# Optimization experiments

Hardware: AMD Instinct MI355X
Metric: run time of the kernel (lower is better)

Reference implementation:

```python
import jax, jax.numpy as jnp
import numpy as np

B, T, U, V = 8, 128, 100, 1024
BLANK = 0
NEG = -1e30  # safe -inf surrogate (finite grads through logaddexp)


def setup_inputs() -> dict:
    key = jax.random.key(0)
    k1, k2 = jax.random.split(key)
    logits = jax.random.normal(k1, (B, T, U + 1, V), dtype=jnp.float32)
    # targets drawn from non-blank ids [1, V)
    targets = jax.random.randint(k2, (B, U), 1, V, dtype=jnp.int32)
    logit_lengths = jnp.full((B,), T, dtype=jnp.int32)
    target_lengths = jnp.full((B,), U, dtype=jnp.int32)
    return {"logits": logits, "targets": targets,
            "logit_lengths": logit_lengths, "target_lengths": target_lengths}


def _rnnt_nll(log_probs, targets, t_len, u_len):
    """Negative log-likelihood of one utterance.
    log_probs: [T, U+1, V] (log-softmaxed joiner output), targets: [U] int.
    alpha[t,u] = logaddexp(alpha[t-1,u] + blank[t-1,u], alpha[t,u-1] + emit[t,u-1]).
    """
    blank_lp = log_probs[:, :, BLANK]                      # [T, U+1]
    emit_lp = log_probs[:, jnp.arange(U), targets]         # [T, U]

    # row t=0: pure emissions
    alpha0 = jnp.concatenate([jnp.zeros((1,), log_probs.dtype),
                              jnp.cumsum(emit_lp[0])])     # [U+1]

    def combine(x, y):
        # linear log-space recurrence x[u] = logaddexp(c[u], x[u-1] + a[u])
        a1, c1 = x
        a2, c2 = y
        return (a1 + a2, jnp.logaddexp(c2, c1 + a2))

    def step(prev_row, inp):
        blank_prev, emit_t = inp                           # [U+1], [U]
        c = prev_row + blank_prev                          # vertical (blank) moves
        a = jnp.concatenate([jnp.full((1,), NEG, log_probs.dtype), emit_t])
        _, row = jax.lax.associative_scan(combine, (a, c))
        return row, row

    _, rows = jax.lax.scan(step, alpha0, (blank_lp[:-1], emit_lp[1:]))
    alpha = jnp.concatenate([alpha0[None, :], rows], axis=0)  # [T, U+1]

    ll = alpha[t_len - 1, u_len] + blank_lp[t_len - 1, u_len]
    return -ll


def reference(logits, targets, logit_lengths, target_lengths):
    log_probs = jax.nn.log_softmax(logits, axis=-1)
    # module passes src_lengths - 1 to rnnt_loss
    t_lens = logit_lengths - 1
    nll = jax.vmap(_rnnt_nll)(log_probs, targets, t_lens, target_lengths)
    return jnp.mean(nll)  # reduction='mean'
```

## Files before the change

kernel.cpp:

```cpp
#include <hip/hip_runtime.h>


constexpr int Bb = 8;
constexpr int Tt = 128;
constexpr int Uu = 100;
constexpr int Vv = 1024;
constexpr int UP1 = Uu + 1;
constexpr int DROWS = 244;
constexpr int PAIRS = 52;
constexpr int ROWB  = PAIRS * 8;
constexpr int LROWS = 233;
constexpr int REG   = 29;
constexpr int NREG  = 8;
constexpr int RBYTES = REG * ROWB;

__device__ __forceinline__ unsigned short f2bf(float f) {
    unsigned int u = __builtin_bit_cast(unsigned int, f);
    u += 0x7fffu + ((u >> 16) & 1u);
    return (unsigned short)(u >> 16);
}
__device__ __forceinline__ float bflo(unsigned int p) {
    return __builtin_bit_cast(float, p << 16);
}
__device__ __forceinline__ float bfhi(unsigned int p) {
    return __builtin_bit_cast(float, p & 0xffff0000u);
}

__device__ __forceinline__ float wave_shr1(float x) {
    return __builtin_bit_cast(float, __builtin_amdgcn_update_dpp(
        0, __builtin_bit_cast(int, x), 0x138, 0xf, 0xf, true));
}
__device__ __forceinline__ float readlane_f(float x, int lane) {
    return __builtin_bit_cast(float,
        __builtin_amdgcn_readlane(__builtin_bit_cast(int, x), lane));
}

#define DPP_MAXSTEP(x, ctrl, rmask) {                                        \
    float _t = __builtin_bit_cast(float, __builtin_amdgcn_update_dpp(        \
        __builtin_bit_cast(int, x), __builtin_bit_cast(int, x),              \
        ctrl, rmask, 0xf, false));                                           \
    x = fmaxf(x, _t); }
#define WAVE_SCAN_MAX(x)           \
    DPP_MAXSTEP(x, 0x111, 0xf);    \
    DPP_MAXSTEP(x, 0x112, 0xf);    \
    DPP_MAXSTEP(x, 0x114, 0xf);    \
    DPP_MAXSTEP(x, 0x118, 0xf);    \
    DPP_MAXSTEP(x, 0x142, 0xa);    \
    DPP_MAXSTEP(x, 0x143, 0xc)

__global__ __launch_bounds__(256) void lse_kernel(
        const float* __restrict__ logits,
        const int*   __restrict__ targets,
        unsigned short* __restrict__ gS,
        int* __restrict__ dcnt) {
    if (blockIdx.x == 0 && threadIdx.x == 0)
        __hip_atomic_store(dcnt, 0, __ATOMIC_RELAXED, __HIP_MEMORY_SCOPE_AGENT);

    const int wid  = blockIdx.x * 4 + (threadIdx.x >> 6);
    const int lane = threadIdx.x & 63;
    const int b   = wid / (Tt * UP1);
    const int rem = wid - b * (Tt * UP1);
    const int t   = rem / UP1;
    const int u   = rem - t * UP1;

    const float* row = logits + (size_t)wid * Vv;
    const float4* r4 = (const float4*)row;
    float4 x0 = r4[lane];
    float4 x1 = r4[lane + 64];
    float4 x2 = r4[lane + 128];
    float4 x3 = r4[lane + 192];

    float m = fmaxf(fmaxf(fmaxf(x0.x, x0.y), fmaxf(x0.z, x0.w)),
                    fmaxf(fmaxf(x1.x, x1.y), fmaxf(x1.z, x1.w)));
    m = fmaxf(m, fmaxf(fmaxf(fmaxf(x2.x, x2.y), fmaxf(x2.z, x2.w)),
                       fmaxf(fmaxf(x3.x, x3.y), fmaxf(x3.z, x3.w))));
    #pragma unroll
    for (int d = 32; d > 0; d >>= 1) m = fmaxf(m, __shfl_xor(m, d, 64));

    float s = __expf(x0.x - m) + __expf(x0.y - m) + __expf(x0.z - m) + __expf(x0.w - m)
            + __expf(x1.x - m) + __expf(x1.y - m) + __expf(x1.z - m) + __expf(x1.w - m)
            + __expf(x2.x - m) + __expf(x2.y - m) + __expf(x2.z - m) + __expf(x2.w - m)
            + __expf(x3.x - m) + __expf(x3.y - m) + __expf(x3.z - m) + __expf(x3.w - m);
    #pragma unroll
    for (int d = 32; d > 0; d >>= 1) s += __shfl_xor(s, d, 64);

    float lse = m + __logf(s);

    if (lane == 0) {
        const int dw = t + u + 1;
        const size_t rowoff = ((size_t)b * DROWS + dw) * (PAIRS * 4);
        gS[rowoff + (u >> 1) * 4 + (u & 1)] = f2bf(__expf(x0.x - lse));
        if (u < Uu) {
            int tgt = targets[b * Uu + u];
            const int sidx = u + 1;
            gS[rowoff + (sidx >> 1) * 4 + 2 + (sidx & 1)] = f2bf(__expf(row[tgt] - lse));
        }
    }
}

__global__ __launch_bounds__(576) void dp_kernel(
        const unsigned short* __restrict__ gS,
        const int* __restrict__ logit_lengths,
        const int* __restrict__ target_lengths,
        float* __restrict__ nll,
        int*   __restrict__ dcnt,
        float* __restrict__ out) {
    const int b    = blockIdx.x;
    const int tid  = threadIdx.x;
    const int wvi  = tid >> 6;
    const int lane = tid & 63;

    __shared__ __align__(16) unsigned short lBE[LROWS][PAIRS][4];
    __shared__ int sflag[NREG];

    if (tid < NREG) sflag[tid] = 0;
    __syncthreads();

    if (wvi >= 1) {
        const int w = wvi - 1;
        const int row0 = 1 + REG * w;
        const char* gb = (const char*)gS + ((size_t)b * DROWS + row0) * ROWB;
        char* db = (char*)lBE + (size_t)row0 * ROWB;

        uint4 v[12];
        #pragma unroll
        for (int i = 0; i < 12; ++i)
            v[i] = *(const uint4*)(gb + lane * 16 + i * 1024);
        #pragma unroll
        for (int i = 0; i < 11; ++i)
            *(uint4*)(db + lane * 16 + i * 1024) = v[i];
        if (lane < 50)
            *(uint4*)(db + lane * 16 + 11 * 1024) = v[11];

        if (lane < REG) {
            const int d = row0 + lane;
            lBE[d][0][2]  = 0;
            lBE[d][50][1] = 0;
            lBE[d][50][3] = 0;
            lBE[d][51][0] = 0; lBE[d][51][1] = 0;
            lBE[d][51][2] = 0; lBE[d][51][3] = 0;
        }
        __hip_atomic_store(&sflag[w], 1, __ATOMIC_RELEASE,
                           __HIP_MEMORY_SCOPE_WORKGROUP);
        return;
    }

    const int tl = logit_lengths[b];
    const int ul = target_lengths[b];
    const int t_idx = tl - 2;
    const int dcap  = t_idx + ul;

    const int lpair = (lane < 51) ? lane : 51;
    const char* lbase = (const char*)lBE + lpair * 8;

    float P0 = (lane == 0) ? 1.0f : 0.0f;
    float P1 = 0.0f;
    float S  = 0.0f;
    float capP0 = (dcap == 0) ? 1.0f : 0.0f, capP1 = 0.0f, capS = 0.0f;

#define PSTEP(dv, w0, w1) do {                                         \
        float Bx = bflo(w0), By = bfhi(w0);                            \
        float Ex = bflo(w1), Ey = bfhi(w1);                            \
        float sh = wave_shr1(P1);                                      \
        float n1 = fmaf(P1, By, P0 * Ey);                              \
        float n0 = fmaf(P0, Bx, sh * Ex);                              \
        P0 = n0; P1 = n1;                                              \
        if ((dv) == dcap) { capP0 = n0; capP1 = n1; capS = S; }        \
    } while (0)

#define RESCALE do {                                                   \
        float gm = fmaxf(P0, P1);                                      \
        WAVE_SCAN_MAX(gm);                                             \
        float mm = fmaxf(readlane_f(gm, 63), 1e-30f);                  \
        float rr = 1.0f / mm;                                          \
        P0 *= rr; P1 *= rr;                                            \
        S += __logf(mm);                                               \
    } while (0)

#define LOADG(UB, UE, k) do {                                          \
        _Pragma("unroll")                                              \
        for (int r = 0; r < 8; ++r) {                                  \
            uint2 q = *(const uint2*)(lbase +                          \
                        (size_t)((k) * 8 + 1 + r) * ROWB);             \
            UB[r] = q.x; UE[r] = q.y;                                  \
        }                                                              \
    } while (0)

#define COMPG(UB, UE, k) do {                                          \
        _Pragma("unroll")                                              \
        for (int r = 0; r < 8; ++r)                                    \
            PSTEP((k) * 8 + 1 + r, UB[r], UE[r]);                      \
        RESCALE;                                                       \
    } while (0)

    int wcur = -1;
#define ENSURE(wn) do {                                                \
        while (wcur < (wn)) {                                          \
            ++wcur;                                                    \
            while (__hip_atomic_load(&sflag[wcur], __ATOMIC_ACQUIRE,   \
                       __HIP_MEMORY_SCOPE_WORKGROUP) == 0)             \
                __builtin_amdgcn_s_sleep(1);                           \
        }                                                              \
    } while (0)

    unsigned int Ab[8], Ae[8], Bb_[8], Be_[8];
    ENSURE(0);
    LOADG(Ab, Ae, 0);
    for (int c = 0; c < 14; ++c) {
        const int k0 = 2 * c, k1 = 2 * c + 1;
        ENSURE((8 * k1 + 7) / REG);
        LOADG(Bb_, Be_, k1);
        COMPG(Ab, Ae, k0);
        if (k1 < 28) {
            ENSURE((8 * (k1 + 1) + 7) / REG);
            LOADG(Ab, Ae, k1 + 1);
        }
        COMPG(Bb_, Be_, k1);
    }
    COMPG(Ab, Ae, 28);
#undef PSTEP
#undef RESCALE
#undef LOADG
#undef COMPG
#undef ENSURE

    float w0 = readlane_f(capP0, ul >> 1);
    float w1 = readlane_f(capP1, ul >> 1);
    float capv = (ul & 1) ? w1 : w0;

    if (lane == 0) {
        unsigned short hv = lBE[dcap + 1][ul >> 1][ul & 1];
        float blk = __builtin_bit_cast(float, ((unsigned int)hv) << 16);
        float ll = __logf(capv) + capS + __logf(blk);
        __hip_atomic_store(&nll[b], -ll, __ATOMIC_RELEASE,
                           __HIP_MEMORY_SCOPE_AGENT);
        int prev = __hip_atomic_fetch_add(dcnt, 1, __ATOMIC_ACQ_REL,
                                          __HIP_MEMORY_SCOPE_AGENT);
        if (prev == Bb - 1) {
            float s = 0.0f;
            for (int i = 0; i < Bb; ++i)
                s += __hip_atomic_load(&nll[i], __ATOMIC_ACQUIRE,
                                       __HIP_MEMORY_SCOPE_AGENT);
            out[0] = s / (float)Bb;
        }
    }
}

extern "C" void kernel_launch(void* const* d_in, const int* in_sizes, int n_in,
                              void* d_out, int out_size, void* d_ws, size_t ws_size,
                              hipStream_t stream) {
    const float* logits         = (const float*)d_in[0];
    const int*   targets        = (const int*)d_in[1];
    const int*   logit_lengths  = (const int*)d_in[2];
    const int*   target_lengths = (const int*)d_in[3];
    float* out = (float*)d_out;

    int* dcnt = (int*)d_ws;
    unsigned short* gS = (unsigned short*)d_ws + 16;
    float* nll = (float*)(gS + (size_t)Bb * DROWS * PAIRS * 4);

    const int rows = Bb * Tt * UP1;
    lse_kernel<<<rows / 4, 256, 0, stream>>>(logits, targets, gS, dcnt);
    dp_kernel<<<Bb, 576, 0, stream>>>(gS, logit_lengths, target_lengths,
                                      nll, dcnt, out);
}
```

Measured before the change: 88.81 us.

## Fuse LSE and DP into one cooperative persistent kernel with grid sync

```diff
diff --git a/kernel.cpp b/kernel.cpp
--- a/kernel.cpp
+++ b/kernel.cpp
@@ -1,4 +1,7 @@
 #include <hip/hip_runtime.h>
+#include <hip/hip_cooperative_groups.h>
+
+namespace cg = cooperative_groups;
 
 
 constexpr int Bb = 8;
@@ -6,13 +9,10 @@
 constexpr int Uu = 100;
 constexpr int Vv = 1024;
 constexpr int UP1 = Uu + 1;
+constexpr int NROWS = Bb * Tt * UP1;
 constexpr int DROWS = 244;
 constexpr int PAIRS = 52;
 constexpr int ROWB  = PAIRS * 8;
-constexpr int LROWS = 233;
-constexpr int REG   = 29;
-constexpr int NREG  = 8;
-constexpr int RBYTES = REG * ROWB;
 
 __device__ __forceinline__ unsigned short f2bf(float f) {
     unsigned int u = __builtin_bit_cast(unsigned int, f);
@@ -48,16 +48,11 @@
     DPP_MAXSTEP(x, 0x142, 0xa);    \
     DPP_MAXSTEP(x, 0x143, 0xc)
 
-__global__ __launch_bounds__(256) void lse_kernel(
+__device__ __forceinline__ void lse_row(
+        int wid, int lane,
         const float* __restrict__ logits,
         const int*   __restrict__ targets,
-        unsigned short* __restrict__ gS,
-        int* __restrict__ dcnt) {
-    if (blockIdx.x == 0 && threadIdx.x == 0)
-        __hip_atomic_store(dcnt, 0, __ATOMIC_RELAXED, __HIP_MEMORY_SCOPE_AGENT);
-
-    const int wid  = blockIdx.x * 4 + (threadIdx.x >> 6);
-    const int lane = threadIdx.x & 63;
+        unsigned short* __restrict__ gS) {
     const int b   = wid / (Tt * UP1);
     const int rem = wid - b * (Tt * UP1);
     const int t   = rem / UP1;
@@ -98,60 +93,21 @@
     }
 }
 
-__global__ __launch_bounds__(576) void dp_kernel(
+__device__ __forceinline__ void dp_consume(
+        int b, int lane,
         const unsigned short* __restrict__ gS,
         const int* __restrict__ logit_lengths,
         const int* __restrict__ target_lengths,
         float* __restrict__ nll,
         int*   __restrict__ dcnt,
         float* __restrict__ out) {
-    const int b    = blockIdx.x;
-    const int tid  = threadIdx.x;
-    const int wvi  = tid >> 6;
-    const int lane = tid & 63;
-
-    __shared__ __align__(16) unsigned short lBE[LROWS][PAIRS][4];
-    __shared__ int sflag[NREG];
-
-    if (tid < NREG) sflag[tid] = 0;
-    __syncthreads();
-
-    if (wvi >= 1) {
-        const int w = wvi - 1;
-        const int row0 = 1 + REG * w;
-        const char* gb = (const char*)gS + ((size_t)b * DROWS + row0) * ROWB;
-        char* db = (char*)lBE + (size_t)row0 * ROWB;
-
-        uint4 v[12];
-        #pragma unroll
-        for (int i = 0; i < 12; ++i)
-            v[i] = *(const uint4*)(gb + lane * 16 + i * 1024);
-        #pragma unroll
-        for (int i = 0; i < 11; ++i)
-            *(uint4*)(db + lane * 16 + i * 1024) = v[i];
-        if (lane < 50)
-            *(uint4*)(db + lane * 16 + 11 * 1024) = v[11];
-
-        if (lane < REG) {
-            const int d = row0 + lane;
-            lBE[d][0][2]  = 0;
-            lBE[d][50][1] = 0;
-            lBE[d][50][3] = 0;
-            lBE[d][51][0] = 0; lBE[d][51][1] = 0;
-            lBE[d][51][2] = 0; lBE[d][51][3] = 0;
-        }
-        __hip_atomic_store(&sflag[w], 1, __ATOMIC_RELEASE,
-                           __HIP_MEMORY_SCOPE_WORKGROUP);
-        return;
-    }
-
     const int tl = logit_lengths[b];
     const int ul = target_lengths[b];
     const int t_idx = tl - 2;
     const int dcap  = t_idx + ul;
 
     const int lpair = (lane < 51) ? lane : 51;
-    const char* lbase = (const char*)lBE + lpair * 8;
+    const char* gbase = (const char*)gS + (size_t)b * DROWS * ROWB + lpair * 8;
 
     float P0 = (lane == 0) ? 1.0f : 0.0f;
     float P1 = 0.0f;
@@ -177,10 +133,10 @@
         S += __logf(mm);                                               \
     } while (0)
 
-#define LOADG(UB, UE, k) do {                                          \
+#define GLOADG(UB, UE, k) do {                                         \
         _Pragma("unroll")                                              \
         for (int r = 0; r < 8; ++r) {                                  \
-            uint2 q = *(const uint2*)(lbase +                          \
+            uint2 q = *(const uint2*)(gbase +                          \
                         (size_t)((k) * 8 + 1 + r) * ROWB);             \
             UB[r] = q.x; UE[r] = q.y;                                  \
         }                                                              \
@@ -193,43 +149,32 @@
         RESCALE;                                                       \
     } while (0)
 
-    int wcur = -1;
-#define ENSURE(wn) do {                                                \
-        while (wcur < (wn)) {                                          \
-            ++wcur;                                                    \
-            while (__hip_atomic_load(&sflag[wcur], __ATOMIC_ACQUIRE,   \
-                       __HIP_MEMORY_SCOPE_WORKGROUP) == 0)             \
-                __builtin_amdgcn_s_sleep(1);                           \
-        }                                                              \
-    } while (0)
-
-    unsigned int Ab[8], Ae[8], Bb_[8], Be_[8];
-    ENSURE(0);
-    LOADG(Ab, Ae, 0);
-    for (int c = 0; c < 14; ++c) {
-        const int k0 = 2 * c, k1 = 2 * c + 1;
-        ENSURE((8 * k1 + 7) / REG);
-        LOADG(Bb_, Be_, k1);
-        COMPG(Ab, Ae, k0);
-        if (k1 < 28) {
-            ENSURE((8 * (k1 + 1) + 7) / REG);
-            LOADG(Ab, Ae, k1 + 1);
-        }
-        COMPG(Bb_, Be_, k1);
-    }
-    COMPG(Ab, Ae, 28);
+    unsigned int Ab[8], Ae[8], Bf[8], Be[8], Cb[8], Ce[8];
+    GLOADG(Ab, Ae, 0);
+    GLOADG(Bf, Be, 1);
+    GLOADG(Cb, Ce, 2);
+    for (int c = 0; c < 9; ++c) {
+        const int k = 3 * c;
+        COMPG(Ab, Ae, k);     if (k + 3 < 29) GLOADG(Ab, Ae, k + 3);
+        COMPG(Bf, Be, k + 1); if (k + 4 < 29) GLOADG(Bf, Be, k + 4);
+        COMPG(Cb, Ce, k + 2); if (k + 5 < 29) GLOADG(Cb, Ce, k + 5);
+    }
+    COMPG(Ab, Ae, 27);
+    COMPG(Bf, Be, 28);
 #undef PSTEP
 #undef RESCALE
-#undef LOADG
+#undef GLOADG
 #undef COMPG
-#undef ENSURE
 
     float w0 = readlane_f(capP0, ul >> 1);
     float w1 = readlane_f(capP1, ul >> 1);
     float capv = (ul & 1) ? w1 : w0;
 
     if (lane == 0) {
-        unsigned short hv = lBE[dcap + 1][ul >> 1][ul & 1];
+        const unsigned short* gb =
+            gS + (size_t)b * DROWS * PAIRS * 4;
+        unsigned short hv = gb[(size_t)(dcap + 1) * PAIRS * 4
+                               + (ul >> 1) * 4 + (ul & 1)];
         float blk = __builtin_bit_cast(float, ((unsigned int)hv) << 16);
         float ll = __logf(capv) + capS + __logf(blk);
         __hip_atomic_store(&nll[b], -ll, __ATOMIC_RELEASE,
@@ -246,6 +191,57 @@
     }
 }
 
+__global__ __launch_bounds__(512) void fused_kernel(
+        const float* __restrict__ logits,
+        const int*   __restrict__ targets,
+        const int*   __restrict__ logit_lengths,
+        const int*   __restrict__ target_lengths,
+        unsigned short* __restrict__ gS,
+        float* __restrict__ nll,
+        int*   __restrict__ dcnt,
+        float* __restrict__ out) {
+    const int tid  = threadIdx.x;
+    const int lane = tid & 63;
+    const int wvi  = tid >> 6;
+
+    if (blockIdx.x == gridDim.x - 1 && tid == 0)
+        __hip_atomic_store(dcnt, 0, __ATOMIC_RELAXED, __HIP_MEMORY_SCOPE_AGENT);
+
+    const int gwaves = gridDim.x * 8;
+    for (int wid = blockIdx.x * 8 + wvi; wid < NROWS; wid += gwaves)
+        lse_row(wid, lane, logits, targets, gS);
+
+    __threadfence();
+    cg::this_grid().sync();
+
+    if (blockIdx.x >= Bb || wvi != 0) return;
+    dp_consume(blockIdx.x, lane, gS, logit_lengths, target_lengths,
+               nll, dcnt, out);
+}
+
+__global__ __launch_bounds__(256) void lse_kernel(
+        const float* __restrict__ logits,
+        const int*   __restrict__ targets,
+        unsigned short* __restrict__ gS,
+        int* __restrict__ dcnt) {
+    if (blockIdx.x == 0 && threadIdx.x == 0)
+        __hip_atomic_store(dcnt, 0, __ATOMIC_RELAXED, __HIP_MEMORY_SCOPE_AGENT);
+    const int wid  = blockIdx.x * 4 + (threadIdx.x >> 6);
+    const int lane = threadIdx.x & 63;
+    lse_row(wid, lane, logits, targets, gS);
+}
+
+__global__ __launch_bounds__(64) void dp_kernel(
+        const unsigned short* __restrict__ gS,
+        const int* __restrict__ logit_lengths,
+        const int* __restrict__ target_lengths,
+        float* __restrict__ nll,
+        int*   __restrict__ dcnt,
+        float* __restrict__ out) {
+    dp_consume(blockIdx.x, threadIdx.x & 63, gS,
+               logit_lengths, target_lengths, nll, dcnt, out);
+}
+
 extern "C" void kernel_launch(void* const* d_in, const int* in_sizes, int n_in,
                               void* d_out, int out_size, void* d_ws, size_t ws_size,
                               hipStream_t stream) {
@@ -259,8 +255,24 @@
     unsigned short* gS = (unsigned short*)d_ws + 16;
     float* nll = (float*)(gS + (size_t)Bb * DROWS * PAIRS * 4);
 
-    const int rows = Bb * Tt * UP1;
-    lse_kernel<<<rows / 4, 256, 0, stream>>>(logits, targets, gS, dcnt);
-    dp_kernel<<<Bb, 576, 0, stream>>>(gS, logit_lengths, target_lengths,
-                                      nll, dcnt, out);
-}
+    int nb = 0;
+    hipOccupancyMaxActiveBlocksPerMultiprocessor(&nb, fused_kernel, 512, 0);
+    int dev = 0;
+    hipGetDevice(&dev);
+    int ncu = 0;
+    hipDeviceGetAttribute(&ncu, hipDeviceAttributeMultiprocessorCount, dev);
+    int grid = nb * ncu;
+    if (grid < Bb) grid = Bb;
+
+    void* args[] = { (void*)&logits, (void*)&targets, (void*)&logit_lengths,
+                     (void*)&target_lengths, (void*)&gS, (void*)&nll,
+                     (void*)&dcnt, (void*)&out };
+    hipError_t err = hipLaunchCooperativeKernel(
+        fused_kernel, dim3(grid), dim3(512), args, 0, stream);
+
+    if (err != hipSuccess) {
+        lse_kernel<<<NROWS / 4, 256, 0, stream>>>(logits, targets, gS, dcnt);
+        dp_kernel<<<Bb, 64, 0, stream>>>(gS, logit_lengths, target_lengths,
+                                         nll, dcnt, out);
+    }
+}
```

Result: slower. 237.6 us (+167.5%).
